# Performance work log

Measured on AMD Instinct MI355X. Metric: run time of the kernel, lower is better.

Reference implementation:

```python
import jax, jax.numpy as jnp
import numpy as np

W = 64   # window_size
S = 1    # window_stride
H = 4    # n_head
D = 64   # head_size


def setup_inputs() -> dict:
    key = jax.random.key(0)
    ks = jax.random.split(key, 6)
    B, T, C = 2, 2048, 256
    x = jax.random.normal(ks[0], (B, T, C), jnp.float32)
    w_kqv = jax.random.normal(ks[1], (3 * H * D, C), jnp.float32) * 0.05
    w_out = jax.random.normal(ks[2], (C, H * D), jnp.float32) * 0.05
    b_out = jax.random.normal(ks[3], (C,), jnp.float32) * 0.05
    q_pos = jax.random.normal(ks[4], (W, H, D), jnp.float32) * 0.05
    v_pos = jax.random.normal(ks[5], (W, H, D), jnp.float32) * 0.05
    return dict(x=x, w_kqv=w_kqv, w_out=w_out, b_out=b_out, q_pos=q_pos, v_pos=v_pos)


def reference(x, w_kqv, w_out, b_out, q_pos, v_pos):
    B, T, C = x.shape
    # qkv projection: (B, T, 3, H, D)
    kqv = (x @ w_kqv.T).reshape(B, T, 3, H, D)
    # zero-pad W*S steps at the front of time (matches F.pad before as_strided)
    xp = jnp.pad(kqv, ((0, 0), (W * S, 0), (0, 0), (0, 0), (0, 0)))
    Tq = T - S  # output rows after the [:, S:] slice
    # window slot w of output row t' reads padded time t' + S*(w+1)
    # (= original token t' + S - S*(W - w), i.e. tokens t-S, t-2S, ..., t-W*S)
    idx = jnp.arange(Tq)[:, None] + S * (jnp.arange(W)[None, :] + 1)  # (Tq, W)
    win = xp[:, idx]  # (B, Tq, W, 3, H, D)
    tk = win[:, :, :, 0]
    tq = win[:, :, :, 1]
    tv = win[:, :, :, 2]
    # per-slot dot (both k and q come from the same strided window, as in the source)
    wei = jnp.einsum('btwhd,btwhd->btwh', tk, tq)
    wei = wei + jnp.einsum('whd,btwhd->btwh', q_pos, tq)  # relative query bias
    wei = wei * (D ** -0.5)  # scale applied AFTER the relative add, as in source
    # flipped-tril causal mask: row i keeps slots w >= W-1-i (all-true for i >= W)
    valid = jnp.arange(W)[None, :] >= (W - 1 - jnp.arange(Tq)[:, None])  # (Tq, W)
    wei = jnp.where(valid[None, :, :, None], wei, -jnp.inf)
    wei = jax.nn.softmax(wei, axis=2)  # softmax over window dim (dim=-2 in torch)
    # dropout omitted (inference / rate 0)
    out = jnp.einsum('btwh,btwhd->bthd', wei, tv)
    out = out + jnp.einsum('btwh,whd->bthd', wei, v_pos)  # relative value bias
    out = out.reshape(B, Tq, H * D)
    out = jnp.pad(out, ((0, 0), (S, 0), (0, 0)))  # re-pad the first S rows with zeros
    y = out @ w_out.T + b_out
    return (y, wei)
```

## Files before the change

### kernel.cpp

```cpp
#include <hip/hip_runtime.h>
#include <hip/hip_bf16.h>
#include <math.h>

#define BB 2
#define TT 2048
#define CC 256
#define HH 4
#define DD 64
#define WW 64
#define TQ 2047
#define NKQ 512
#define N_KQV 768

typedef __attribute__((ext_vector_type(8))) short bf16x8;
typedef __attribute__((ext_vector_type(4))) float f32x4;
typedef __attribute__((ext_vector_type(4))) unsigned short u16x4;

__device__ inline short f2bf(float x) {
    unsigned u = __float_as_uint(x);
    u += 0x7FFF + ((u >> 16) & 1);
    return (short)(u >> 16);
}
__device__ inline float bf2f(short s) {
    return __uint_as_float(((unsigned)(unsigned short)s) << 16);
}
__device__ inline bf16x8 cvt8(float4 a, float4 b) {
    bf16x8 r;
    r[0] = f2bf(a.x); r[1] = f2bf(a.y); r[2] = f2bf(a.z); r[3] = f2bf(a.w);
    r[4] = f2bf(b.x); r[5] = f2bf(b.y); r[6] = f2bf(b.z); r[7] = f2bf(b.w);
    return r;
}

__global__ __launch_bounds__(256)
void gemm_kqv(const float* __restrict__ Av, const float* __restrict__ Bv,
              short* __restrict__ kqb, short* __restrict__ vTb,
              const float* __restrict__ qposf, const float* __restrict__ vposf,
              const float* __restrict__ woutf,
              short* __restrict__ qposb, short* __restrict__ vposTb,
              short* __restrict__ woutb) {
    constexpr int BM = 64, BN = 64, BK = 64, LDA = BK + 8;
    constexpr int MR = 2, NR = 2;
    __shared__ short As[BM][LDA];
    __shared__ short Bs[BN][LDA];

    const int tid = threadIdx.x;

    if ((int)blockIdx.x == 64) {
        const int base = blockIdx.y * 8192;
#pragma unroll
        for (int i = 0; i < 32; ++i) {
            int e = base + i * 256 + tid;
            if (e < 65536) {
                woutb[e] = f2bf(woutf[e]);
            } else if (e < 81920) {
                int e2 = e - 65536;
                int h = e2 >> 12, r = e2 & 4095, w = r >> 6, d = r & 63;
                qposb[e2] = f2bf(qposf[(w * HH + h) * DD + d]);
            } else {
                int e3 = e - 81920;
                int h = e3 >> 12, r = e3 & 4095, d = r >> 6, w = r & 63;
                vposTb[e3] = f2bf(vposf[(w * HH + h) * DD + d]);
            }
        }
        return;
    }

    const int m0 = blockIdx.x * BM, n0 = blockIdx.y * BN;
    const int wv = tid >> 6, lane = tid & 63;
    const int wr = wv >> 1, wc = wv & 1;
    const int col = lane & 15, kg = lane >> 4;

    f32x4 acc[MR][NR];
#pragma unroll
    for (int i = 0; i < MR; ++i)
#pragma unroll
        for (int j = 0; j < NR; ++j) acc[i][j] = (f32x4){0.f, 0.f, 0.f, 0.f};

    for (int k0 = 0; k0 < 256; k0 += BK) {
#pragma unroll
        for (int it = 0; it < 2; ++it) {
            int fi = tid + it * 256;
            int r = fi >> 3, c8 = (fi & 7) << 3;
            const float* ap = Av + (size_t)(m0 + r) * 256 + k0 + c8;
            float4 v0 = *reinterpret_cast<const float4*>(ap);
            float4 v1 = *reinterpret_cast<const float4*>(ap + 4);
            *reinterpret_cast<bf16x8*>(&As[r][c8]) = cvt8(v0, v1);
        }
#pragma unroll
        for (int it = 0; it < 2; ++it) {
            int fi = tid + it * 256;
            int r = fi >> 3, c8 = (fi & 7) << 3;
            const float* bp = Bv + (size_t)(n0 + r) * 256 + k0 + c8;
            float4 v0 = *reinterpret_cast<const float4*>(bp);
            float4 v1 = *reinterpret_cast<const float4*>(bp + 4);
            *reinterpret_cast<bf16x8*>(&Bs[r][c8]) = cvt8(v0, v1);
        }
        __syncthreads();

#pragma unroll
        for (int kk = 0; kk < 2; ++kk) {
            bf16x8 af[MR], bfr[NR];
#pragma unroll
            for (int i = 0; i < MR; ++i)
                af[i] = *reinterpret_cast<const bf16x8*>(
                    &As[wr * 32 + i * 16 + col][kk * 32 + kg * 8]);
#pragma unroll
            for (int j = 0; j < NR; ++j)
                bfr[j] = *reinterpret_cast<const bf16x8*>(
                    &Bs[wc * 32 + j * 16 + col][kk * 32 + kg * 8]);
#pragma unroll
            for (int i = 0; i < MR; ++i)
#pragma unroll
                for (int j = 0; j < NR; ++j)
                    acc[i][j] = __builtin_amdgcn_mfma_f32_16x16x32_bf16(
                        af[i], bfr[j], acc[i][j], 0, 0, 0);
        }
        __syncthreads();
    }

    if (n0 < NKQ) {
#pragma unroll
        for (int i = 0; i < MR; ++i)
#pragma unroll
            for (int j = 0; j < NR; ++j)
#pragma unroll
                for (int r = 0; r < 4; ++r) {
                    int m = m0 + wr * 32 + i * 16 + kg * 4 + r;
                    int n = n0 + wc * 32 + j * 16 + col;
                    kqb[(size_t)m * NKQ + n] = f2bf(acc[i][j][r]);
                }
    } else {
        const int h = (n0 - NKQ) >> 6;
#pragma unroll
        for (int i = 0; i < MR; ++i) {
#pragma unroll
            for (int j = 0; j < NR; ++j) {
                int dloc = wc * 32 + j * 16 + col;
                int m = m0 + wr * 32 + i * 16 + kg * 4;
                int bb = m >> 11, t = m & (TT - 1);
                u16x4 pk;
#pragma unroll
                for (int r = 0; r < 4; ++r) pk[r] = (unsigned short)f2bf(acc[i][j][r]);
                *reinterpret_cast<u16x4*>(
                    vTb + ((size_t)(bb * HH + h) * DD + dloc) * TT + t) = pk;
            }
        }
    }
}

__global__ __launch_bounds__(512)
void attn_fused(const short* __restrict__ kqb, const short* __restrict__ vTb,
                const short* __restrict__ qposb, const short* __restrict__ vposTb,
                float* __restrict__ wei_out, short* __restrict__ attnSb) {
    __shared__ __align__(16) short QS[128 * 72];
    __shared__ __align__(16) short VT[64 * 152];
    __shared__ __align__(16) short PP[4 * 16 * 104];
    __shared__ __align__(16) short PD[4 * 16 * 72];
    __shared__ float SB[64 * 68];
    __shared__ float PT[128 * 9];
    __shared__ float DQ[128];

    const int tid  = threadIdx.x;
    const int wv   = tid >> 6;
    const int lane = tid & 63;
    const int col  = lane & 15;
    const int kg   = lane >> 4;
    const int bid  = blockIdx.x;
    const int tile = bid & 31;
    const int h    = (bid >> 5) & 3;
    const int b    = bid >> 7;
    const int t0   = tile * 64;
    const int j0   = t0 - 63;
    const int j0v  = t0 - 64;

    {
        unsigned int* pz = reinterpret_cast<unsigned int*>(PP);
#pragma unroll
        for (int i = 0; i < 7; ++i) {
            int fi = tid + i * 512;
            if (fi < 3328) pz[fi] = 0u;
        }
    }
#pragma unroll
    for (int it = 0; it < 2; ++it) {
        int fi = tid + it * 512;
        int r = fi >> 3, c8 = (fi & 7) << 3;
        int j = j0 + r;
        bf16x8 kv = (bf16x8){0,0,0,0,0,0,0,0};
        bf16x8 qv = (bf16x8){0,0,0,0,0,0,0,0};
        if (j >= 0 && j < TT) {
            const short* base = kqb + (size_t)(b * TT + j) * NKQ + h * DD + c8;
            kv = *reinterpret_cast<const bf16x8*>(base);
            qv = *reinterpret_cast<const bf16x8*>(base + 256);
        }
        *reinterpret_cast<bf16x8*>(&QS[r * 72 + c8]) = qv;
        float s = 0.f;
#pragma unroll
        for (int q = 0; q < 8; ++q) s += bf2f(kv[q]) * bf2f(qv[q]);
        PT[r * 9 + (fi & 7)] = s;
    }
#pragma unroll
    for (int it = 0; it < 3; ++it) {
        int fi = tid + it * 512;
        if (fi < 1152) {
            int r = fi / 18, c = fi % 18;
            int jl8 = c * 8;
            int j = j0v + jl8;
            bf16x8 v = (bf16x8){0,0,0,0,0,0,0,0};
            if (j >= 0 && j + 7 < TT)
                v = *reinterpret_cast<const bf16x8*>(
                    vTb + ((size_t)(b * HH + h) * DD + r) * TT + j);
            *reinterpret_cast<bf16x8*>(&VT[r * 152 + jl8]) = v;
        }
    }
    __syncthreads();

    if (tid < 128) {
        float s = 0.f;
#pragma unroll
        for (int g = 0; g < 8; ++g) s += PT[tid * 9 + g];
        DQ[tid] = s;
    }
    {
        f32x4 qa[4];
#pragma unroll
        for (int n = 0; n < 4; ++n) qa[n] = (f32x4){0.f, 0.f, 0.f, 0.f};
#pragma unroll
        for (int ks = 0; ks < 2; ++ks) {
            bf16x8 af = *reinterpret_cast<const bf16x8*>(
                &QS[(wv * 16 + col) * 72 + ks * 32 + kg * 8]);
#pragma unroll
            for (int n = 0; n < 4; ++n) {
                bf16x8 bfr = *reinterpret_cast<const bf16x8*>(
                    qposb + h * 4096 + (n * 16 + col) * 64 + ks * 32 + kg * 8);
                qa[n] = __builtin_amdgcn_mfma_f32_16x16x32_bf16(af, bfr, qa[n], 0, 0, 0);
            }
        }
#pragma unroll
        for (int n = 0; n < 4; ++n) {
            int w = n * 16 + col;
#pragma unroll
            for (int r = 0; r < 4; ++r) {
                int jl = wv * 16 + kg * 4 + r;
                int il = jl - w;
                if (il >= 0 && il < 64) SB[il * 68 + w] = qa[n][r];
            }
        }
    }
    __syncthreads();

#pragma unroll
    for (int i2 = 0; i2 < 2; ++i2) {
        int row = wv * 8 + i2 * 4 + kg;
        int t = t0 + row;
        f32x4 sv = *reinterpret_cast<const f32x4*>(&SB[row * 68 + col * 4]);
        float s4[4];
#pragma unroll
        for (int q = 0; q < 4; ++q) {
            int w = col * 4 + q;
            float s = (sv[q] + DQ[row + w]) * 0.125f;
            if (tile == 0 && row + w < 63) s = -INFINITY;
            s4[q] = s;
        }
        float m = fmaxf(fmaxf(s4[0], s4[1]), fmaxf(s4[2], s4[3]));
#pragma unroll
        for (int off = 8; off; off >>= 1) m = fmaxf(m, __shfl_xor(m, off));
        float p[4], sum = 0.f;
#pragma unroll
        for (int q = 0; q < 4; ++q) { p[q] = __expf(s4[q] - m); sum += p[q]; }
#pragma unroll
        for (int off = 8; off; off >>= 1) sum += __shfl_xor(sum, off);
        float inv = 1.f / sum;
        int rg = row >> 4, i16 = row & 15;
        short* pph = PP + rg * 1664;
        short* pdh = PD + rg * 1152;
#pragma unroll
        for (int q = 0; q < 4; ++q) {
            int w = col * 4 + q;
            float wei = p[q] * inv;
            if (t < TQ)
                wei_out[(((size_t)b * TQ + t) * WW + w) * HH + h] = wei;
            short wb = f2bf(wei);
            pdh[i16 * 72 + w] = wb;
            pph[i16 * 104 + i16 + w + 1] = wb;
        }
    }
    __syncthreads();

    {
        const int rg = wv & 3;
        const short* pph = PP + rg * 1664;
        const short* pdh = PD + rg * 1152;
#pragma unroll
        for (int dt2 = 0; dt2 < 2; ++dt2) {
            int dt = (wv >> 2) * 2 + dt2;
            f32x4 pa = (f32x4){0.f, 0.f, 0.f, 0.f};
#pragma unroll
            for (int ks = 0; ks < 3; ++ks) {
                bf16x8 af = *reinterpret_cast<const bf16x8*>(
                    &pph[col * 104 + ks * 32 + kg * 8]);
                bf16x8 bfr = *reinterpret_cast<const bf16x8*>(
                    &VT[(dt * 16 + col) * 152 + rg * 16 + ks * 32 + kg * 8]);
                pa = __builtin_amdgcn_mfma_f32_16x16x32_bf16(af, bfr, pa, 0, 0, 0);
            }
#pragma unroll
            for (int ks = 0; ks < 2; ++ks) {
                bf16x8 af = *reinterpret_cast<const bf16x8*>(
                    &pdh[col * 72 + ks * 32 + kg * 8]);
                bf16x8 bfr = *reinterpret_cast<const bf16x8*>(
                    vposTb + h * 4096 + (dt * 16 + col) * 64 + ks * 32 + kg * 8);
                pa = __builtin_amdgcn_mfma_f32_16x16x32_bf16(af, bfr, pa, 0, 0, 0);
            }
#pragma unroll
            for (int r = 0; r < 4; ++r) {
                int t = t0 + rg * 16 + kg * 4 + r;
                if (t < TQ)
                    attnSb[((size_t)(b * TT) + t + 1) * CC + h * DD + dt * 16 + col] =
                        f2bf(pa[r]);
            }
        }
    }
}

__global__ __launch_bounds__(256)
void gemm_out(const short* __restrict__ Ab, const short* __restrict__ Bb,
              const float* __restrict__ bias, float* __restrict__ C) {
    constexpr int BM = 32, BN = 64, BK = 64, LDA = BK + 8;
    constexpr int NR = 2;
    __shared__ short As[BM][LDA];
    __shared__ short Bs[BN][LDA];

    const int tid = threadIdx.x;
    const int m0 = blockIdx.x * BM, n0 = blockIdx.y * BN;
    const int wv = tid >> 6, lane = tid & 63;
    const int wr = wv >> 1, wc = wv & 1;
    const int col = lane & 15, kg = lane >> 4;

    f32x4 acc[NR];
#pragma unroll
    for (int j = 0; j < NR; ++j) acc[j] = (f32x4){0.f, 0.f, 0.f, 0.f};

    for (int k0 = 0; k0 < 256; k0 += BK) {
        {
            int fi = tid;
            int r = fi >> 3, c8 = (fi & 7) << 3;
            int gr = m0 + r;
            bf16x8 sv = (bf16x8){0,0,0,0,0,0,0,0};
            if ((gr & (TT - 1)) != 0)
                sv = *reinterpret_cast<const bf16x8*>(Ab + (size_t)gr * 256 + k0 + c8);
            *reinterpret_cast<bf16x8*>(&As[r][c8]) = sv;
        }
#pragma unroll
        for (int it = 0; it < 2; ++it) {
            int fi = tid + it * 256;
            int r = fi >> 3, c8 = (fi & 7) << 3;
            *reinterpret_cast<bf16x8*>(&Bs[r][c8]) =
                *reinterpret_cast<const bf16x8*>(Bb + (size_t)(n0 + r) * 256 + k0 + c8);
        }
        __syncthreads();

#pragma unroll
        for (int kk = 0; kk < 2; ++kk) {
            bf16x8 af = *reinterpret_cast<const bf16x8*>(
                &As[wr * 16 + col][kk * 32 + kg * 8]);
#pragma unroll
            for (int j = 0; j < NR; ++j) {
                bf16x8 bfr = *reinterpret_cast<const bf16x8*>(
                    &Bs[wc * 32 + j * 16 + col][kk * 32 + kg * 8]);
                acc[j] = __builtin_amdgcn_mfma_f32_16x16x32_bf16(af, bfr, acc[j], 0, 0, 0);
            }
        }
        __syncthreads();
    }

#pragma unroll
    for (int j = 0; j < NR; ++j)
#pragma unroll
        for (int r = 0; r < 4; ++r) {
            int m = m0 + wr * 16 + kg * 4 + r;
            int n = n0 + wc * 32 + j * 16 + col;
            C[(size_t)m * 256 + n] = acc[j][r] + bias[n];
        }
}

extern "C" void kernel_launch(void* const* d_in, const int* in_sizes, int n_in,
                              void* d_out, int out_size, void* d_ws, size_t ws_size,
                              hipStream_t stream) {
    const float* x     = (const float*)d_in[0];
    const float* w_kqv = (const float*)d_in[1];
    const float* w_out = (const float*)d_in[2];
    const float* b_out = (const float*)d_in[3];
    const float* q_pos = (const float*)d_in[4];
    const float* v_pos = (const float*)d_in[5];

    float* y   = (float*)d_out;
    float* wei = (float*)d_out + (size_t)BB * TT * CC;

    short* kqb    = (short*)d_ws;
    short* vTb    = kqb + (size_t)BB * TT * NKQ;
    short* woutb  = vTb + (size_t)BB * HH * DD * TT;
    short* qposb  = woutb + 65536;
    short* vposTb = qposb + 16384;
    short* attnSb = vposTb + 16384;

    gemm_kqv<<<dim3(65, 12), 256, 0, stream>>>(
        x, w_kqv, kqb, vTb, q_pos, v_pos, w_out, qposb, vposTb, woutb);

    attn_fused<<<BB * HH * 32, 512, 0, stream>>>(
        kqb, vTb, qposb, vposTb, wei, attnSb);

    gemm_out<<<dim3((BB * TT) / 32, CC / 64), 256, 0, stream>>>(
        attnSb, woutb, b_out, y);
}
```

Before: 37.66 us.

## Fuse three kernels into one cooperative persistent kernel with grid syncs

Replaces the QKV GEMM, attention and output GEMM launches with a single cooperative kernel of 256 blocks that separates the phases with grid.sync(). V is no longer stored transposed in global memory. It is written row-major with K and Q and transposed into LDS inside the attention phase. The aim is to remove launch gaps and inter-kernel tails. The cost is reduced parallelism in the GEMM phases, where each block now does larger tiles (64x192, and 16 rows by the full 256 columns), plus the overhead of the grid barriers.

```diff
diff --git a/kernel.cpp b/kernel.cpp
--- a/kernel.cpp
+++ b/kernel.cpp
@@ -1,4 +1,5 @@
 #include <hip/hip_runtime.h>
+#include <hip/hip_cooperative_groups.h>
 #include <hip/hip_bf16.h>
 #include <math.h>
 
@@ -9,12 +10,12 @@
 #define DD 64
 #define WW 64
 #define TQ 2047
-#define NKQ 512
-#define N_KQV 768
+#define NKV 768
+
+namespace cg = cooperative_groups;
 
 typedef __attribute__((ext_vector_type(8))) short bf16x8;
 typedef __attribute__((ext_vector_type(4))) float f32x4;
-typedef __attribute__((ext_vector_type(4))) unsigned short u16x4;
 
 __device__ inline short f2bf(float x) {
     unsigned u = __float_as_uint(x);
@@ -31,134 +32,18 @@
     return r;
 }
 
-__global__ __launch_bounds__(256)
-void gemm_kqv(const float* __restrict__ Av, const float* __restrict__ Bv,
-              short* __restrict__ kqb, short* __restrict__ vTb,
-              const float* __restrict__ qposf, const float* __restrict__ vposf,
-              const float* __restrict__ woutf,
-              short* __restrict__ qposb, short* __restrict__ vposTb,
-              short* __restrict__ woutb) {
-    constexpr int BM = 64, BN = 64, BK = 64, LDA = BK + 8;
-    constexpr int MR = 2, NR = 2;
-    __shared__ short As[BM][LDA];
-    __shared__ short Bs[BN][LDA];
-
-    const int tid = threadIdx.x;
-
-    if ((int)blockIdx.x == 64) {
-        const int base = blockIdx.y * 8192;
-#pragma unroll
-        for (int i = 0; i < 32; ++i) {
-            int e = base + i * 256 + tid;
-            if (e < 65536) {
-                woutb[e] = f2bf(woutf[e]);
-            } else if (e < 81920) {
-                int e2 = e - 65536;
-                int h = e2 >> 12, r = e2 & 4095, w = r >> 6, d = r & 63;
-                qposb[e2] = f2bf(qposf[(w * HH + h) * DD + d]);
-            } else {
-                int e3 = e - 81920;
-                int h = e3 >> 12, r = e3 & 4095, d = r >> 6, w = r & 63;
-                vposTb[e3] = f2bf(vposf[(w * HH + h) * DD + d]);
-            }
-        }
-        return;
-    }
-
-    const int m0 = blockIdx.x * BM, n0 = blockIdx.y * BN;
-    const int wv = tid >> 6, lane = tid & 63;
-    const int wr = wv >> 1, wc = wv & 1;
-    const int col = lane & 15, kg = lane >> 4;
-
-    f32x4 acc[MR][NR];
-#pragma unroll
-    for (int i = 0; i < MR; ++i)
-#pragma unroll
-        for (int j = 0; j < NR; ++j) acc[i][j] = (f32x4){0.f, 0.f, 0.f, 0.f};
-
-    for (int k0 = 0; k0 < 256; k0 += BK) {
-#pragma unroll
-        for (int it = 0; it < 2; ++it) {
-            int fi = tid + it * 256;
-            int r = fi >> 3, c8 = (fi & 7) << 3;
-            const float* ap = Av + (size_t)(m0 + r) * 256 + k0 + c8;
-            float4 v0 = *reinterpret_cast<const float4*>(ap);
-            float4 v1 = *reinterpret_cast<const float4*>(ap + 4);
-            *reinterpret_cast<bf16x8*>(&As[r][c8]) = cvt8(v0, v1);
-        }
-#pragma unroll
-        for (int it = 0; it < 2; ++it) {
-            int fi = tid + it * 256;
-            int r = fi >> 3, c8 = (fi & 7) << 3;
-            const float* bp = Bv + (size_t)(n0 + r) * 256 + k0 + c8;
-            float4 v0 = *reinterpret_cast<const float4*>(bp);
-            float4 v1 = *reinterpret_cast<const float4*>(bp + 4);
-            *reinterpret_cast<bf16x8*>(&Bs[r][c8]) = cvt8(v0, v1);
-        }
-        __syncthreads();
-
-#pragma unroll
-        for (int kk = 0; kk < 2; ++kk) {
-            bf16x8 af[MR], bfr[NR];
-#pragma unroll
-            for (int i = 0; i < MR; ++i)
-                af[i] = *reinterpret_cast<const bf16x8*>(
-                    &As[wr * 32 + i * 16 + col][kk * 32 + kg * 8]);
-#pragma unroll
-            for (int j = 0; j < NR; ++j)
-                bfr[j] = *reinterpret_cast<const bf16x8*>(
-                    &Bs[wc * 32 + j * 16 + col][kk * 32 + kg * 8]);
-#pragma unroll
-            for (int i = 0; i < MR; ++i)
-#pragma unroll
-                for (int j = 0; j < NR; ++j)
-                    acc[i][j] = __builtin_amdgcn_mfma_f32_16x16x32_bf16(
-                        af[i], bfr[j], acc[i][j], 0, 0, 0);
-        }
-        __syncthreads();
-    }
-
-    if (n0 < NKQ) {
-#pragma unroll
-        for (int i = 0; i < MR; ++i)
-#pragma unroll
-            for (int j = 0; j < NR; ++j)
-#pragma unroll
-                for (int r = 0; r < 4; ++r) {
-                    int m = m0 + wr * 32 + i * 16 + kg * 4 + r;
-                    int n = n0 + wc * 32 + j * 16 + col;
-                    kqb[(size_t)m * NKQ + n] = f2bf(acc[i][j][r]);
-                }
-    } else {
-        const int h = (n0 - NKQ) >> 6;
-#pragma unroll
-        for (int i = 0; i < MR; ++i) {
-#pragma unroll
-            for (int j = 0; j < NR; ++j) {
-                int dloc = wc * 32 + j * 16 + col;
-                int m = m0 + wr * 32 + i * 16 + kg * 4;
-                int bb = m >> 11, t = m & (TT - 1);
-                u16x4 pk;
-#pragma unroll
-                for (int r = 0; r < 4; ++r) pk[r] = (unsigned short)f2bf(acc[i][j][r]);
-                *reinterpret_cast<u16x4*>(
-                    vTb + ((size_t)(bb * HH + h) * DD + dloc) * TT + t) = pk;
-            }
-        }
-    }
-}
+#define LDS_SHORTS 41472
 
 __global__ __launch_bounds__(512)
-void attn_fused(const short* __restrict__ kqb, const short* __restrict__ vTb,
-                const short* __restrict__ qposb, const short* __restrict__ vposTb,
-                float* __restrict__ wei_out, short* __restrict__ attnSb) {
-    __shared__ __align__(16) short QS[128 * 72];
-    __shared__ __align__(16) short VT[64 * 152];
-    __shared__ __align__(16) short PP[4 * 16 * 104];
-    __shared__ __align__(16) short PD[4 * 16 * 72];
-    __shared__ float SB[64 * 68];
-    __shared__ float PT[128 * 9];
-    __shared__ float DQ[128];
+void mega(const float* __restrict__ x, const float* __restrict__ w_kqv,
+          const float* __restrict__ w_out, const float* __restrict__ b_out,
+          const float* __restrict__ q_pos, const float* __restrict__ v_pos,
+          float* __restrict__ y, float* __restrict__ wei_out,
+          short* __restrict__ kqvb, short* __restrict__ qposb,
+          short* __restrict__ vposTb, short* __restrict__ woutb,
+          short* __restrict__ attnSb) {
+    __shared__ __align__(16) short lds[LDS_SHORTS];
+    cg::grid_group grid = cg::this_grid();
 
     const int tid  = threadIdx.x;
     const int wv   = tid >> 6;
@@ -166,221 +51,309 @@
     const int col  = lane & 15;
     const int kg   = lane >> 4;
     const int bid  = blockIdx.x;
-    const int tile = bid & 31;
-    const int h    = (bid >> 5) & 3;
-    const int b    = bid >> 7;
-    const int t0   = tile * 64;
-    const int j0   = t0 - 63;
-    const int j0v  = t0 - 64;
 
     {
-        unsigned int* pz = reinterpret_cast<unsigned int*>(PP);
-#pragma unroll
-        for (int i = 0; i < 7; ++i) {
-            int fi = tid + i * 512;
-            if (fi < 3328) pz[fi] = 0u;
+        const int m0 = (bid >> 2) * 64, n0 = (bid & 3) * 192;
+        const int wr = wv >> 2, wc = wv & 3;
+        short* As = lds;
+        short* Bs = lds + 4608;
+
+        f32x4 acc[2][3];
+#pragma unroll
+        for (int i = 0; i < 2; ++i)
+#pragma unroll
+            for (int j = 0; j < 3; ++j) acc[i][j] = (f32x4){0.f, 0.f, 0.f, 0.f};
+
+        for (int k0 = 0; k0 < 256; k0 += 64) {
+            {
+                int r = tid >> 3, c8 = (tid & 7) << 3;
+                const float* ap = x + (size_t)(m0 + r) * 256 + k0 + c8;
+                float4 v0 = *reinterpret_cast<const float4*>(ap);
+                float4 v1 = *reinterpret_cast<const float4*>(ap + 4);
+                *reinterpret_cast<bf16x8*>(&As[r * 72 + c8]) = cvt8(v0, v1);
+            }
+#pragma unroll
+            for (int it = 0; it < 3; ++it) {
+                int fi = tid + it * 512;
+                int r = fi >> 3, c8 = (fi & 7) << 3;
+                const float* bp = w_kqv + (size_t)(n0 + r) * 256 + k0 + c8;
+                float4 v0 = *reinterpret_cast<const float4*>(bp);
+                float4 v1 = *reinterpret_cast<const float4*>(bp + 4);
+                *reinterpret_cast<bf16x8*>(&Bs[r * 72 + c8]) = cvt8(v0, v1);
+            }
+            __syncthreads();
+#pragma unroll
+            for (int kk = 0; kk < 2; ++kk) {
+                bf16x8 af[2], bfr[3];
+#pragma unroll
+                for (int i = 0; i < 2; ++i)
+                    af[i] = *reinterpret_cast<const bf16x8*>(
+                        &As[(wr * 32 + i * 16 + col) * 72 + kk * 32 + kg * 8]);
+#pragma unroll
+                for (int j = 0; j < 3; ++j)
+                    bfr[j] = *reinterpret_cast<const bf16x8*>(
+                        &Bs[(wc * 48 + j * 16 + col) * 72 + kk * 32 + kg * 8]);
+#pragma unroll
+                for (int i = 0; i < 2; ++i)
+#pragma unroll
+                    for (int j = 0; j < 3; ++j)
+                        acc[i][j] = __builtin_amdgcn_mfma_f32_16x16x32_bf16(
+                            af[i], bfr[j], acc[i][j], 0, 0, 0);
+            }
+            __syncthreads();
+        }
+#pragma unroll
+        for (int i = 0; i < 2; ++i)
+#pragma unroll
+            for (int j = 0; j < 3; ++j)
+#pragma unroll
+                for (int r = 0; r < 4; ++r) {
+                    int m = m0 + wr * 32 + i * 16 + kg * 4 + r;
+                    int n = n0 + wc * 48 + j * 16 + col;
+                    kqvb[(size_t)m * NKV + n] = f2bf(acc[i][j][r]);
+                }
+
+        if (bid < 8) {
+            const int base = bid * 12288;
+#pragma unroll
+            for (int i = 0; i < 24; ++i) {
+                int e = base + i * 512 + tid;
+                if (e < 65536) {
+                    woutb[e] = f2bf(w_out[e]);
+                } else if (e < 81920) {
+                    int e2 = e - 65536;
+                    int h = e2 >> 12, rr = e2 & 4095, w = rr >> 6, d = rr & 63;
+                    qposb[e2] = f2bf(q_pos[(w * HH + h) * DD + d]);
+                } else {
+                    int e3 = e - 81920;
+                    int h = e3 >> 12, rr = e3 & 4095, d = rr >> 6, w = rr & 63;
+                    vposTb[e3] = f2bf(v_pos[(w * HH + h) * DD + d]);
+                }
+            }
         }
     }
-#pragma unroll
-    for (int it = 0; it < 2; ++it) {
-        int fi = tid + it * 512;
-        int r = fi >> 3, c8 = (fi & 7) << 3;
-        int j = j0 + r;
-        bf16x8 kv = (bf16x8){0,0,0,0,0,0,0,0};
-        bf16x8 qv = (bf16x8){0,0,0,0,0,0,0,0};
-        if (j >= 0 && j < TT) {
-            const short* base = kqb + (size_t)(b * TT + j) * NKQ + h * DD + c8;
-            kv = *reinterpret_cast<const bf16x8*>(base);
-            qv = *reinterpret_cast<const bf16x8*>(base + 256);
-        }
-        *reinterpret_cast<bf16x8*>(&QS[r * 72 + c8]) = qv;
-        float s = 0.f;
-#pragma unroll
-        for (int q = 0; q < 8; ++q) s += bf2f(kv[q]) * bf2f(qv[q]);
-        PT[r * 9 + (fi & 7)] = s;
-    }
-#pragma unroll
-    for (int it = 0; it < 3; ++it) {
-        int fi = tid + it * 512;
-        if (fi < 1152) {
-            int r = fi / 18, c = fi % 18;
-            int jl8 = c * 8;
-            int j = j0v + jl8;
-            bf16x8 v = (bf16x8){0,0,0,0,0,0,0,0};
-            if (j >= 0 && j + 7 < TT)
-                v = *reinterpret_cast<const bf16x8*>(
-                    vTb + ((size_t)(b * HH + h) * DD + r) * TT + j);
-            *reinterpret_cast<bf16x8*>(&VT[r * 152 + jl8]) = v;
-        }
-    }
-    __syncthreads();
-
-    if (tid < 128) {
-        float s = 0.f;
-#pragma unroll
-        for (int g = 0; g < 8; ++g) s += PT[tid * 9 + g];
-        DQ[tid] = s;
-    }
+    grid.sync();
+
     {
-        f32x4 qa[4];
-#pragma unroll
-        for (int n = 0; n < 4; ++n) qa[n] = (f32x4){0.f, 0.f, 0.f, 0.f};
-#pragma unroll
-        for (int ks = 0; ks < 2; ++ks) {
-            bf16x8 af = *reinterpret_cast<const bf16x8*>(
-                &QS[(wv * 16 + col) * 72 + ks * 32 + kg * 8]);
-#pragma unroll
-            for (int n = 0; n < 4; ++n) {
-                bf16x8 bfr = *reinterpret_cast<const bf16x8*>(
-                    qposb + h * 4096 + (n * 16 + col) * 64 + ks * 32 + kg * 8);
-                qa[n] = __builtin_amdgcn_mfma_f32_16x16x32_bf16(af, bfr, qa[n], 0, 0, 0);
-            }
-        }
-#pragma unroll
-        for (int n = 0; n < 4; ++n) {
-            int w = n * 16 + col;
-#pragma unroll
-            for (int r = 0; r < 4; ++r) {
-                int jl = wv * 16 + kg * 4 + r;
-                int il = jl - w;
-                if (il >= 0 && il < 64) SB[il * 68 + w] = qa[n][r];
-            }
-        }
-    }
-    __syncthreads();
-
-#pragma unroll
-    for (int i2 = 0; i2 < 2; ++i2) {
-        int row = wv * 8 + i2 * 4 + kg;
-        int t = t0 + row;
-        f32x4 sv = *reinterpret_cast<const f32x4*>(&SB[row * 68 + col * 4]);
-        float s4[4];
-#pragma unroll
-        for (int q = 0; q < 4; ++q) {
-            int w = col * 4 + q;
-            float s = (sv[q] + DQ[row + w]) * 0.125f;
-            if (tile == 0 && row + w < 63) s = -INFINITY;
-            s4[q] = s;
-        }
-        float m = fmaxf(fmaxf(s4[0], s4[1]), fmaxf(s4[2], s4[3]));
-#pragma unroll
-        for (int off = 8; off; off >>= 1) m = fmaxf(m, __shfl_xor(m, off));
-        float p[4], sum = 0.f;
-#pragma unroll
-        for (int q = 0; q < 4; ++q) { p[q] = __expf(s4[q] - m); sum += p[q]; }
-#pragma unroll
-        for (int off = 8; off; off >>= 1) sum += __shfl_xor(sum, off);
-        float inv = 1.f / sum;
-        int rg = row >> 4, i16 = row & 15;
-        short* pph = PP + rg * 1664;
-        short* pdh = PD + rg * 1152;
-#pragma unroll
-        for (int q = 0; q < 4; ++q) {
-            int w = col * 4 + q;
-            float wei = p[q] * inv;
-            if (t < TQ)
-                wei_out[(((size_t)b * TQ + t) * WW + w) * HH + h] = wei;
-            short wb = f2bf(wei);
-            pdh[i16 * 72 + w] = wb;
-            pph[i16 * 104 + i16 + w + 1] = wb;
-        }
-    }
-    __syncthreads();
-
-    {
-        const int rg = wv & 3;
-        const short* pph = PP + rg * 1664;
-        const short* pdh = PD + rg * 1152;
-#pragma unroll
-        for (int dt2 = 0; dt2 < 2; ++dt2) {
-            int dt = (wv >> 2) * 2 + dt2;
-            f32x4 pa = (f32x4){0.f, 0.f, 0.f, 0.f};
-#pragma unroll
-            for (int ks = 0; ks < 3; ++ks) {
-                bf16x8 af = *reinterpret_cast<const bf16x8*>(
-                    &pph[col * 104 + ks * 32 + kg * 8]);
-                bf16x8 bfr = *reinterpret_cast<const bf16x8*>(
-                    &VT[(dt * 16 + col) * 152 + rg * 16 + ks * 32 + kg * 8]);
-                pa = __builtin_amdgcn_mfma_f32_16x16x32_bf16(af, bfr, pa, 0, 0, 0);
-            }
+        short* QS = lds;
+        short* VT = lds + 9216;
+        short* PP = lds + 18944;
+        short* PD = lds + 25600;
+        float* fb = reinterpret_cast<float*>(lds + 30208);
+        float* SB = fb;
+        float* PT = fb + 4352;
+        float* DQ = fb + 5504;
+
+        const int tile = bid & 31;
+        const int h    = (bid >> 5) & 3;
+        const int b    = bid >> 7;
+        const int t0   = tile * 64;
+        const int j0   = t0 - 63;
+        const int j0v  = t0 - 64;
+        const short* kqv_b = kqvb + (size_t)(b * TT) * NKV;
+
+        {
+            unsigned int* pz = reinterpret_cast<unsigned int*>(PP);
+#pragma unroll
+            for (int i = 0; i < 7; ++i) {
+                int fi = tid + i * 512;
+                if (fi < 3328) pz[fi] = 0u;
+            }
+        }
+#pragma unroll
+        for (int it = 0; it < 2; ++it) {
+            int fi = tid + it * 512;
+            int r = fi >> 3, c8 = (fi & 7) << 3;
+            int j = j0 + r;
+            bf16x8 kv = (bf16x8){0,0,0,0,0,0,0,0};
+            bf16x8 qv = (bf16x8){0,0,0,0,0,0,0,0};
+            if (j >= 0 && j < TT) {
+                const short* base = kqv_b + (size_t)j * NKV + h * DD + c8;
+                kv = *reinterpret_cast<const bf16x8*>(base);
+                qv = *reinterpret_cast<const bf16x8*>(base + 256);
+            }
+            *reinterpret_cast<bf16x8*>(&QS[r * 72 + c8]) = qv;
+            float s = 0.f;
+#pragma unroll
+            for (int q = 0; q < 8; ++q) s += bf2f(kv[q]) * bf2f(qv[q]);
+            PT[r * 9 + (fi & 7)] = s;
+        }
+#pragma unroll
+        for (int it = 0; it < 3; ++it) {
+            int fi = tid + it * 512;
+            if (fi < 1216) {
+                int r = fi >> 3, c = fi & 7, c8 = c << 3;
+                int j = j0v + r;
+                bf16x8 v = (bf16x8){0,0,0,0,0,0,0,0};
+                if (r < 144 && j >= 0 && j < TT)
+                    v = *reinterpret_cast<const bf16x8*>(
+                        kqv_b + (size_t)j * NKV + 512 + h * DD + c8);
+#pragma unroll
+                for (int q0 = 0; q0 < 8; ++q0) {
+                    int qp = (q0 + c) & 7;
+                    VT[(c8 + qp) * 152 + r] = v[qp];
+                }
+            }
+        }
+        __syncthreads();
+
+        if (tid < 128) {
+            float s = 0.f;
+#pragma unroll
+            for (int g = 0; g < 8; ++g) s += PT[tid * 9 + g];
+            DQ[tid] = s;
+        }
+        {
+            f32x4 qa[4];
+#pragma unroll
+            for (int n = 0; n < 4; ++n) qa[n] = (f32x4){0.f, 0.f, 0.f, 0.f};
 #pragma unroll
             for (int ks = 0; ks < 2; ++ks) {
                 bf16x8 af = *reinterpret_cast<const bf16x8*>(
-                    &pdh[col * 72 + ks * 32 + kg * 8]);
-                bf16x8 bfr = *reinterpret_cast<const bf16x8*>(
-                    vposTb + h * 4096 + (dt * 16 + col) * 64 + ks * 32 + kg * 8);
-                pa = __builtin_amdgcn_mfma_f32_16x16x32_bf16(af, bfr, pa, 0, 0, 0);
-            }
+                    &QS[(wv * 16 + col) * 72 + ks * 32 + kg * 8]);
+#pragma unroll
+                for (int n = 0; n < 4; ++n) {
+                    bf16x8 bfr = *reinterpret_cast<const bf16x8*>(
+                        qposb + h * 4096 + (n * 16 + col) * 64 + ks * 32 + kg * 8);
+                    qa[n] = __builtin_amdgcn_mfma_f32_16x16x32_bf16(af, bfr, qa[n], 0, 0, 0);
+                }
+            }
+#pragma unroll
+            for (int n = 0; n < 4; ++n) {
+                int w = n * 16 + col;
+#pragma unroll
+                for (int r = 0; r < 4; ++r) {
+                    int jl = wv * 16 + kg * 4 + r;
+                    int il = jl - w;
+                    if (il >= 0 && il < 64) SB[il * 68 + w] = qa[n][r];
+                }
+            }
+        }
+        __syncthreads();
+
+#pragma unroll
+        for (int i2 = 0; i2 < 2; ++i2) {
+            int row = wv * 8 + i2 * 4 + kg;
+            int t = t0 + row;
+            f32x4 sv = *reinterpret_cast<const f32x4*>(&SB[row * 68 + col * 4]);
+            float s4[4];
+#pragma unroll
+            for (int q = 0; q < 4; ++q) {
+                int w = col * 4 + q;
+                float s = (sv[q] + DQ[row + w]) * 0.125f;
+                if (tile == 0 && row + w < 63) s = -INFINITY;
+                s4[q] = s;
+            }
+            float m = fmaxf(fmaxf(s4[0], s4[1]), fmaxf(s4[2], s4[3]));
+#pragma unroll
+            for (int off = 8; off; off >>= 1) m = fmaxf(m, __shfl_xor(m, off));
+            float p[4], sum = 0.f;
+#pragma unroll
+            for (int q = 0; q < 4; ++q) { p[q] = __expf(s4[q] - m); sum += p[q]; }
+#pragma unroll
+            for (int off = 8; off; off >>= 1) sum += __shfl_xor(sum, off);
+            float inv = 1.f / sum;
+            int rg = row >> 4, i16 = row & 15;
+            short* pph = PP + rg * 1664;
+            short* pdh = PD + rg * 1152;
+#pragma unroll
+            for (int q = 0; q < 4; ++q) {
+                int w = col * 4 + q;
+                float wei = p[q] * inv;
+                if (t < TQ)
+                    wei_out[(((size_t)b * TQ + t) * WW + w) * HH + h] = wei;
+                short wb = f2bf(wei);
+                pdh[i16 * 72 + w] = wb;
+                pph[i16 * 104 + i16 + w + 1] = wb;
+            }
+        }
+        __syncthreads();
+
+        {
+            const int rg = wv & 3;
+            const short* pph = PP + rg * 1664;
+            const short* pdh = PD + rg * 1152;
+#pragma unroll
+            for (int dt2 = 0; dt2 < 2; ++dt2) {
+                int dt = (wv >> 2) * 2 + dt2;
+                f32x4 pa = (f32x4){0.f, 0.f, 0.f, 0.f};
+#pragma unroll
+                for (int ks = 0; ks < 3; ++ks) {
+                    bf16x8 af = *reinterpret_cast<const bf16x8*>(
+                        &pph[col * 104 + ks * 32 + kg * 8]);
+                    bf16x8 bfr = *reinterpret_cast<const bf16x8*>(
+                        &VT[(dt * 16 + col) * 152 + rg * 16 + ks * 32 + kg * 8]);
+                    pa = __builtin_amdgcn_mfma_f32_16x16x32_bf16(af, bfr, pa, 0, 0, 0);
+                }
+#pragma unroll
+                for (int ks = 0; ks < 2; ++ks) {
+                    bf16x8 af = *reinterpret_cast<const bf16x8*>(
+                        &pdh[col * 72 + ks * 32 + kg * 8]);
+                    bf16x8 bfr = *reinterpret_cast<const bf16x8*>(
+                        vposTb + h * 4096 + (dt * 16 + col) * 64 + ks * 32 + kg * 8);
+                    pa = __builtin_amdgcn_mfma_f32_16x16x32_bf16(af, bfr, pa, 0, 0, 0);
+                }
+#pragma unroll
+                for (int r = 0; r < 4; ++r) {
+                    int t = t0 + rg * 16 + kg * 4 + r;
+                    if (t < TQ)
+                        attnSb[((size_t)(b * TT) + t + 1) * CC + h * DD + dt * 16 + col] =
+                            f2bf(pa[r]);
+                }
+            }
+        }
+    }
+    grid.sync();
+
+    {
+        short* As = lds;
+        short* Bs = lds + 1152;
+        const int m0 = bid * 16;
+
+        f32x4 acc[2];
+#pragma unroll
+        for (int j = 0; j < 2; ++j) acc[j] = (f32x4){0.f, 0.f, 0.f, 0.f};
+
+        for (int k0 = 0; k0 < 256; k0 += 64) {
+            if (tid < 128) {
+                int r = tid >> 3, c8 = (tid & 7) << 3;
+                int gr = m0 + r;
+                bf16x8 sv = (bf16x8){0,0,0,0,0,0,0,0};
+                if ((gr & (TT - 1)) != 0)
+                    sv = *reinterpret_cast<const bf16x8*>(
+                        attnSb + (size_t)gr * 256 + k0 + c8);
+                *reinterpret_cast<bf16x8*>(&As[r * 72 + c8]) = sv;
+            }
+#pragma unroll
+            for (int it = 0; it < 4; ++it) {
+                int fi = tid + it * 512;
+                int r = fi >> 3, c8 = (fi & 7) << 3;
+                *reinterpret_cast<bf16x8*>(&Bs[r * 72 + c8]) =
+                    *reinterpret_cast<const bf16x8*>(woutb + (size_t)r * 256 + k0 + c8);
+            }
+            __syncthreads();
+#pragma unroll
+            for (int kk = 0; kk < 2; ++kk) {
+                bf16x8 af = *reinterpret_cast<const bf16x8*>(
+                    &As[col * 72 + kk * 32 + kg * 8]);
+#pragma unroll
+                for (int j = 0; j < 2; ++j) {
+                    bf16x8 bfr = *reinterpret_cast<const bf16x8*>(
+                        &Bs[(wv * 32 + j * 16 + col) * 72 + kk * 32 + kg * 8]);
+                    acc[j] = __builtin_amdgcn_mfma_f32_16x16x32_bf16(af, bfr, acc[j], 0, 0, 0);
+                }
+            }
+            __syncthreads();
+        }
+#pragma unroll
+        for (int j = 0; j < 2; ++j)
 #pragma unroll
             for (int r = 0; r < 4; ++r) {
-                int t = t0 + rg * 16 + kg * 4 + r;
-                if (t < TQ)
-                    attnSb[((size_t)(b * TT) + t + 1) * CC + h * DD + dt * 16 + col] =
-                        f2bf(pa[r]);
-            }
-        }
+                int m = m0 + kg * 4 + r;
+                int n = wv * 32 + j * 16 + col;
+                y[(size_t)m * 256 + n] = acc[j][r] + b_out[n];
+            }
     }
-}
-
-__global__ __launch_bounds__(256)
-void gemm_out(const short* __restrict__ Ab, const short* __restrict__ Bb,
-              const float* __restrict__ bias, float* __restrict__ C) {
-    constexpr int BM = 32, BN = 64, BK = 64, LDA = BK + 8;
-    constexpr int NR = 2;
-    __shared__ short As[BM][LDA];
-    __shared__ short Bs[BN][LDA];
-
-    const int tid = threadIdx.x;
-    const int m0 = blockIdx.x * BM, n0 = blockIdx.y * BN;
-    const int wv = tid >> 6, lane = tid & 63;
-    const int wr = wv >> 1, wc = wv & 1;
-    const int col = lane & 15, kg = lane >> 4;
-
-    f32x4 acc[NR];
-#pragma unroll
-    for (int j = 0; j < NR; ++j) acc[j] = (f32x4){0.f, 0.f, 0.f, 0.f};
-
-    for (int k0 = 0; k0 < 256; k0 += BK) {
-        {
-            int fi = tid;
-            int r = fi >> 3, c8 = (fi & 7) << 3;
-            int gr = m0 + r;
-            bf16x8 sv = (bf16x8){0,0,0,0,0,0,0,0};
-            if ((gr & (TT - 1)) != 0)
-                sv = *reinterpret_cast<const bf16x8*>(Ab + (size_t)gr * 256 + k0 + c8);
-            *reinterpret_cast<bf16x8*>(&As[r][c8]) = sv;
-        }
-#pragma unroll
-        for (int it = 0; it < 2; ++it) {
-            int fi = tid + it * 256;
-            int r = fi >> 3, c8 = (fi & 7) << 3;
-            *reinterpret_cast<bf16x8*>(&Bs[r][c8]) =
-                *reinterpret_cast<const bf16x8*>(Bb + (size_t)(n0 + r) * 256 + k0 + c8);
-        }
-        __syncthreads();
-
-#pragma unroll
-        for (int kk = 0; kk < 2; ++kk) {
-            bf16x8 af = *reinterpret_cast<const bf16x8*>(
-                &As[wr * 16 + col][kk * 32 + kg * 8]);
-#pragma unroll
-            for (int j = 0; j < NR; ++j) {
-                bf16x8 bfr = *reinterpret_cast<const bf16x8*>(
-                    &Bs[wc * 32 + j * 16 + col][kk * 32 + kg * 8]);
-                acc[j] = __builtin_amdgcn_mfma_f32_16x16x32_bf16(af, bfr, acc[j], 0, 0, 0);
-            }
-        }
-        __syncthreads();
-    }
-
-#pragma unroll
-    for (int j = 0; j < NR; ++j)
-#pragma unroll
-        for (int r = 0; r < 4; ++r) {
-            int m = m0 + wr * 16 + kg * 4 + r;
-            int n = n0 + wc * 32 + j * 16 + col;
-            C[(size_t)m * 256 + n] = acc[j][r] + bias[n];
-        }
 }
 
 extern "C" void kernel_launch(void* const* d_in, const int* in_sizes, int n_in,
@@ -396,19 +369,18 @@
     float* y   = (float*)d_out;
     float* wei = (float*)d_out + (size_t)BB * TT * CC;
 
-    short* kqb    = (short*)d_ws;
-    short* vTb    = kqb + (size_t)BB * TT * NKQ;
-    short* woutb  = vTb + (size_t)BB * HH * DD * TT;
+    short* kqvb   = (short*)d_ws;
+    short* woutb  = kqvb + (size_t)BB * TT * NKV;
     short* qposb  = woutb + 65536;
     short* vposTb = qposb + 16384;
     short* attnSb = vposTb + 16384;
 
-    gemm_kqv<<<dim3(65, 12), 256, 0, stream>>>(
-        x, w_kqv, kqb, vTb, q_pos, v_pos, w_out, qposb, vposTb, woutb);
-
-    attn_fused<<<BB * HH * 32, 512, 0, stream>>>(
-        kqb, vTb, qposb, vposTb, wei, attnSb);
-
-    gemm_out<<<dim3((BB * TT) / 32, CC / 64), 256, 0, stream>>>(
-        attnSb, woutb, b_out, y);
-}
+    void* kargs[] = {
+        (void*)&x, (void*)&w_kqv, (void*)&w_out, (void*)&b_out,
+        (void*)&q_pos, (void*)&v_pos, (void*)&y, (void*)&wei,
+        (void*)&kqvb, (void*)&qposb, (void*)&vposTb, (void*)&woutb,
+        (void*)&attnSb
+    };
+    (void)hipLaunchCooperativeKernel((void*)mega, dim3(256), dim3(512),
+                                     kargs, 0, stream);
+}
```

Measured after the change: 119.6 us. 218% more time.

## Store V row-major in unified KQV buffer and transpose into LDS in attention

Applied to the files above, without the earlier changes.

The QKV GEMM now writes a single row-major bf16 KQV buffer, using 96-wide N tiles instead of 64, so the launch grid shrinks from 12 to 8 column blocks. The separate transposed V write path is removed. The attention kernel now loads V rows directly and transposes them into shared memory with a rotated scatter to reduce bank conflicts. This trades strided global transpose stores for in-LDS scalar scatter stores, and packs the shared arrays into one buffer.

```diff
diff --git a/kernel.cpp b/kernel.cpp
--- a/kernel.cpp
+++ b/kernel.cpp
@@ -9,12 +9,10 @@
 #define DD 64
 #define WW 64
 #define TQ 2047
-#define NKQ 512
-#define N_KQV 768
+#define NKV 768
 
 typedef __attribute__((ext_vector_type(8))) short bf16x8;
 typedef __attribute__((ext_vector_type(4))) float f32x4;
-typedef __attribute__((ext_vector_type(4))) unsigned short u16x4;
 
 __device__ inline short f2bf(float x) {
     unsigned u = __float_as_uint(x);
@@ -33,22 +31,21 @@
 
 __global__ __launch_bounds__(256)
 void gemm_kqv(const float* __restrict__ Av, const float* __restrict__ Bv,
-              short* __restrict__ kqb, short* __restrict__ vTb,
+              short* __restrict__ Cb,
               const float* __restrict__ qposf, const float* __restrict__ vposf,
               const float* __restrict__ woutf,
               short* __restrict__ qposb, short* __restrict__ vposTb,
               short* __restrict__ woutb) {
-    constexpr int BM = 64, BN = 64, BK = 64, LDA = BK + 8;
-    constexpr int MR = 2, NR = 2;
+    constexpr int BM = 64, BN = 96, LDA = 72;
     __shared__ short As[BM][LDA];
     __shared__ short Bs[BN][LDA];
 
     const int tid = threadIdx.x;
 
     if ((int)blockIdx.x == 64) {
-        const int base = blockIdx.y * 8192;
-#pragma unroll
-        for (int i = 0; i < 32; ++i) {
+        const int base = blockIdx.y * 12288;
+#pragma unroll
+        for (int i = 0; i < 48; ++i) {
             int e = base + i * 256 + tid;
             if (e < 65536) {
                 woutb[e] = f2bf(woutf[e]);
@@ -70,13 +67,13 @@
     const int wr = wv >> 1, wc = wv & 1;
     const int col = lane & 15, kg = lane >> 4;
 
-    f32x4 acc[MR][NR];
-#pragma unroll
-    for (int i = 0; i < MR; ++i)
-#pragma unroll
-        for (int j = 0; j < NR; ++j) acc[i][j] = (f32x4){0.f, 0.f, 0.f, 0.f};
-
-    for (int k0 = 0; k0 < 256; k0 += BK) {
+    f32x4 acc[2][3];
+#pragma unroll
+    for (int i = 0; i < 2; ++i)
+#pragma unroll
+        for (int j = 0; j < 3; ++j) acc[i][j] = (f32x4){0.f, 0.f, 0.f, 0.f};
+
+    for (int k0 = 0; k0 < 256; k0 += 64) {
 #pragma unroll
         for (int it = 0; it < 2; ++it) {
             int fi = tid + it * 256;
@@ -87,7 +84,7 @@
             *reinterpret_cast<bf16x8*>(&As[r][c8]) = cvt8(v0, v1);
         }
 #pragma unroll
-        for (int it = 0; it < 2; ++it) {
+        for (int it = 0; it < 3; ++it) {
             int fi = tid + it * 256;
             int r = fi >> 3, c8 = (fi & 7) << 3;
             const float* bp = Bv + (size_t)(n0 + r) * 256 + k0 + c8;
@@ -99,66 +96,52 @@
 
 #pragma unroll
         for (int kk = 0; kk < 2; ++kk) {
-            bf16x8 af[MR], bfr[NR];
-#pragma unroll
-            for (int i = 0; i < MR; ++i)
+            bf16x8 af[2], bfr[3];
+#pragma unroll
+            for (int i = 0; i < 2; ++i)
                 af[i] = *reinterpret_cast<const bf16x8*>(
                     &As[wr * 32 + i * 16 + col][kk * 32 + kg * 8]);
 #pragma unroll
-            for (int j = 0; j < NR; ++j)
+            for (int j = 0; j < 3; ++j)
                 bfr[j] = *reinterpret_cast<const bf16x8*>(
-                    &Bs[wc * 32 + j * 16 + col][kk * 32 + kg * 8]);
-#pragma unroll
-            for (int i = 0; i < MR; ++i)
-#pragma unroll
-                for (int j = 0; j < NR; ++j)
+                    &Bs[wc * 48 + j * 16 + col][kk * 32 + kg * 8]);
+#pragma unroll
+            for (int i = 0; i < 2; ++i)
+#pragma unroll
+                for (int j = 0; j < 3; ++j)
                     acc[i][j] = __builtin_amdgcn_mfma_f32_16x16x32_bf16(
                         af[i], bfr[j], acc[i][j], 0, 0, 0);
         }
         __syncthreads();
     }
 
-    if (n0 < NKQ) {
-#pragma unroll
-        for (int i = 0; i < MR; ++i)
-#pragma unroll
-            for (int j = 0; j < NR; ++j)
-#pragma unroll
-                for (int r = 0; r < 4; ++r) {
-                    int m = m0 + wr * 32 + i * 16 + kg * 4 + r;
-                    int n = n0 + wc * 32 + j * 16 + col;
-                    kqb[(size_t)m * NKQ + n] = f2bf(acc[i][j][r]);
-                }
-    } else {
-        const int h = (n0 - NKQ) >> 6;
-#pragma unroll
-        for (int i = 0; i < MR; ++i) {
-#pragma unroll
-            for (int j = 0; j < NR; ++j) {
-                int dloc = wc * 32 + j * 16 + col;
-                int m = m0 + wr * 32 + i * 16 + kg * 4;
-                int bb = m >> 11, t = m & (TT - 1);
-                u16x4 pk;
-#pragma unroll
-                for (int r = 0; r < 4; ++r) pk[r] = (unsigned short)f2bf(acc[i][j][r]);
-                *reinterpret_cast<u16x4*>(
-                    vTb + ((size_t)(bb * HH + h) * DD + dloc) * TT + t) = pk;
-            }
-        }
-    }
-}
+#pragma unroll
+    for (int i = 0; i < 2; ++i)
+#pragma unroll
+        for (int j = 0; j < 3; ++j)
+#pragma unroll
+            for (int r = 0; r < 4; ++r) {
+                int m = m0 + wr * 32 + i * 16 + kg * 4 + r;
+                int n = n0 + wc * 48 + j * 16 + col;
+                Cb[(size_t)m * NKV + n] = f2bf(acc[i][j][r]);
+            }
+}
+
+#define LDS_SHORTS 41472
 
 __global__ __launch_bounds__(512)
-void attn_fused(const short* __restrict__ kqb, const short* __restrict__ vTb,
-                const short* __restrict__ qposb, const short* __restrict__ vposTb,
-                float* __restrict__ wei_out, short* __restrict__ attnSb) {
-    __shared__ __align__(16) short QS[128 * 72];
-    __shared__ __align__(16) short VT[64 * 152];
-    __shared__ __align__(16) short PP[4 * 16 * 104];
-    __shared__ __align__(16) short PD[4 * 16 * 72];
-    __shared__ float SB[64 * 68];
-    __shared__ float PT[128 * 9];
-    __shared__ float DQ[128];
+void attn_fused(const short* __restrict__ kqvb, const short* __restrict__ qposb,
+                const short* __restrict__ vposTb, float* __restrict__ wei_out,
+                short* __restrict__ attnSb) {
+    __shared__ __align__(16) short lds[LDS_SHORTS];
+    short* QS = lds;
+    short* VT = lds + 9216;
+    short* PP = lds + 18944;
+    short* PD = lds + 25600;
+    float* fb = reinterpret_cast<float*>(lds + 30208);
+    float* SB = fb;
+    float* PT = fb + 4352;
+    float* DQ = fb + 5504;
 
     const int tid  = threadIdx.x;
     const int wv   = tid >> 6;
@@ -172,6 +155,7 @@
     const int t0   = tile * 64;
     const int j0   = t0 - 63;
     const int j0v  = t0 - 64;
+    const short* kqv_b = kqvb + (size_t)(b * TT) * NKV;
 
     {
         unsigned int* pz = reinterpret_cast<unsigned int*>(PP);
@@ -189,7 +173,7 @@
         bf16x8 kv = (bf16x8){0,0,0,0,0,0,0,0};
         bf16x8 qv = (bf16x8){0,0,0,0,0,0,0,0};
         if (j >= 0 && j < TT) {
-            const short* base = kqb + (size_t)(b * TT + j) * NKQ + h * DD + c8;
+            const short* base = kqv_b + (size_t)j * NKV + h * DD + c8;
             kv = *reinterpret_cast<const bf16x8*>(base);
             qv = *reinterpret_cast<const bf16x8*>(base + 256);
         }
@@ -203,14 +187,17 @@
     for (int it = 0; it < 3; ++it) {
         int fi = tid + it * 512;
         if (fi < 1152) {
-            int r = fi / 18, c = fi % 18;
-            int jl8 = c * 8;
-            int j = j0v + jl8;
+            int r = fi >> 3, c = fi & 7, c8 = c << 3;
+            int j = j0v + r;
             bf16x8 v = (bf16x8){0,0,0,0,0,0,0,0};
-            if (j >= 0 && j + 7 < TT)
+            if (j >= 0 && j < TT)
                 v = *reinterpret_cast<const bf16x8*>(
-                    vTb + ((size_t)(b * HH + h) * DD + r) * TT + j);
-            *reinterpret_cast<bf16x8*>(&VT[r * 152 + jl8]) = v;
+                    kqv_b + (size_t)j * NKV + 512 + h * DD + c8);
+#pragma unroll
+            for (int q0 = 0; q0 < 8; ++q0) {
+                int qp = (q0 + c) & 7;
+                VT[(c8 + qp) * 152 + r] = v[qp];
+            }
         }
     }
     __syncthreads();
@@ -325,8 +312,7 @@
 __global__ __launch_bounds__(256)
 void gemm_out(const short* __restrict__ Ab, const short* __restrict__ Bb,
               const float* __restrict__ bias, float* __restrict__ C) {
-    constexpr int BM = 32, BN = 64, BK = 64, LDA = BK + 8;
-    constexpr int NR = 2;
+    constexpr int BM = 32, BN = 64, LDA = 72;
     __shared__ short As[BM][LDA];
     __shared__ short Bs[BN][LDA];
 
@@ -336,14 +322,13 @@
     const int wr = wv >> 1, wc = wv & 1;
     const int col = lane & 15, kg = lane >> 4;
 
-    f32x4 acc[NR];
-#pragma unroll
-    for (int j = 0; j < NR; ++j) acc[j] = (f32x4){0.f, 0.f, 0.f, 0.f};
-
-    for (int k0 = 0; k0 < 256; k0 += BK) {
+    f32x4 acc[2];
+#pragma unroll
+    for (int j = 0; j < 2; ++j) acc[j] = (f32x4){0.f, 0.f, 0.f, 0.f};
+
+    for (int k0 = 0; k0 < 256; k0 += 64) {
         {
-            int fi = tid;
-            int r = fi >> 3, c8 = (fi & 7) << 3;
+            int r = tid >> 3, c8 = (tid & 7) << 3;
             int gr = m0 + r;
             bf16x8 sv = (bf16x8){0,0,0,0,0,0,0,0};
             if ((gr & (TT - 1)) != 0)
@@ -364,7 +349,7 @@
             bf16x8 af = *reinterpret_cast<const bf16x8*>(
                 &As[wr * 16 + col][kk * 32 + kg * 8]);
 #pragma unroll
-            for (int j = 0; j < NR; ++j) {
+            for (int j = 0; j < 2; ++j) {
                 bf16x8 bfr = *reinterpret_cast<const bf16x8*>(
                     &Bs[wc * 32 + j * 16 + col][kk * 32 + kg * 8]);
                 acc[j] = __builtin_amdgcn_mfma_f32_16x16x32_bf16(af, bfr, acc[j], 0, 0, 0);
@@ -374,7 +359,7 @@
     }
 
 #pragma unroll
-    for (int j = 0; j < NR; ++j)
+    for (int j = 0; j < 2; ++j)
 #pragma unroll
         for (int r = 0; r < 4; ++r) {
             int m = m0 + wr * 16 + kg * 4 + r;
@@ -396,18 +381,17 @@
     float* y   = (float*)d_out;
     float* wei = (float*)d_out + (size_t)BB * TT * CC;
 
-    short* kqb    = (short*)d_ws;
-    short* vTb    = kqb + (size_t)BB * TT * NKQ;
-    short* woutb  = vTb + (size_t)BB * HH * DD * TT;
+    short* kqvb   = (short*)d_ws;
+    short* woutb  = kqvb + (size_t)BB * TT * NKV;
     short* qposb  = woutb + 65536;
     short* vposTb = qposb + 16384;
     short* attnSb = vposTb + 16384;
 
-    gemm_kqv<<<dim3(65, 12), 256, 0, stream>>>(
-        x, w_kqv, kqb, vTb, q_pos, v_pos, w_out, qposb, vposTb, woutb);
+    gemm_kqv<<<dim3(65, 8), 256, 0, stream>>>(
+        x, w_kqv, kqvb, q_pos, v_pos, w_out, qposb, vposTb, woutb);
 
     attn_fused<<<BB * HH * 32, 512, 0, stream>>>(
-        kqb, vTb, qposb, vposTb, wei, attnSb);
+        kqvb, qposb, vposTb, wei, attnSb);
 
     gemm_out<<<dim3((BB * TT) / 32, CC / 64), 256, 0, stream>>>(
         attnSb, woutb, b_out, y);
```

Measured after the change: 42.83 us. 13.8% more time.
